# Kernel tuning notes

Measured on AMD Instinct MI355X. Metric: run time of the kernel, lower is better.

Reference implementation:

```python
import jax, jax.numpy as jnp
import numpy as np

H = 16
D = 1024
DK = D // H


def setup_inputs() -> dict:
    key = jax.random.key(0)
    ks = jax.random.split(key, 10)
    B, S = 2, 2048
    scale = 1.0 / np.sqrt(D)
    inp = {
        "query": jax.random.normal(ks[0], (B, S, D), jnp.float32),
        "key_": jax.random.normal(ks[1], (B, S, D), jnp.float32),
        "value": jax.random.normal(ks[2], (B, S, D), jnp.float32),
        "Wq": jax.random.normal(ks[3], (D, D), jnp.float32) * scale,
        "bq": jnp.zeros((D,), jnp.float32),
        "Wk": jax.random.normal(ks[4], (D, D), jnp.float32) * scale,
        "bk": jnp.zeros((D,), jnp.float32),
        "Wv": jax.random.normal(ks[5], (D, D), jnp.float32) * scale,
        "bv": jnp.zeros((D,), jnp.float32),
        "ln_gamma": jnp.ones((D,), jnp.float32),
        "ln_beta": jnp.zeros((D,), jnp.float32),
    }
    return inp


def reference(query, key_, value, Wq, bq, Wk, bk, Wv, bv, ln_gamma, ln_beta):
    B, S, _ = query.shape
    residual = query
    # projections, split into heads: [B, H, S, DK]
    def proj(x, W, b):
        return (x @ W + b).reshape(B, -1, H, DK).transpose(0, 2, 1, 3)
    q = proj(query, Wq, bq)
    k = proj(key_, Wk, bk)
    v = proj(value, Wv, bv)
    # scaled dot-product attention with full score matrix (as in source)
    scores = jnp.einsum("bhqd,bhkd->bhqk", q, k) / jnp.sqrt(jnp.float32(DK))
    p_att = jax.nn.softmax(scores, axis=-1)  # dropout p=0 -> identity
    x = jnp.einsum("bhqk,bhkd->bhqd", p_att, v)
    x = x.transpose(0, 2, 1, 3).reshape(B, S, D)
    # residual + LayerNorm(eps=1e-6)
    y = x + residual
    mu = jnp.mean(y, axis=-1, keepdims=True)
    var = jnp.var(y, axis=-1, keepdims=True)
    y = (y - mu) / jnp.sqrt(var + 1e-6)
    return y * ln_gamma + ln_beta
```

## Files before the change

### kernel.cpp

```cpp
#include <hip/hip_runtime.h>


typedef float f32x4 __attribute__((ext_vector_type(4)));
typedef short short8 __attribute__((ext_vector_type(8)));
typedef unsigned int uint32x2 __attribute__((ext_vector_type(2)));

__device__ __forceinline__ unsigned short f2bf(float f) {
    unsigned u = __builtin_bit_cast(unsigned, f);
    u += 0x7fffu + ((u >> 16) & 1u);
    return (unsigned short)(u >> 16);
}
__device__ __forceinline__ unsigned packbf2(float lo, float hi) {
    return __builtin_amdgcn_perm(__builtin_bit_cast(unsigned, hi),
                                 __builtin_bit_cast(unsigned, lo), 0x07060302u);
}

__device__ __forceinline__ void g2l16(const unsigned short* g, unsigned short* l) {
    __builtin_amdgcn_global_load_lds(
        (const __attribute__((address_space(1))) unsigned int*)g,
        (__attribute__((address_space(3))) unsigned int*)l, 16, 0, 0);
}

__global__ __launch_bounds__(256) void convert_x(
    const float* __restrict__ xq, const float* __restrict__ xk, const float* __restrict__ xv,
    unsigned short* __restrict__ out)
{
    const int z = blockIdx.z;
    const float* src = (z == 0) ? xq : (z == 1) ? xk : xv;
    const size_t idx = ((size_t)blockIdx.x * 256 + threadIdx.x) * 8;
    const float4 a = *(const float4*)(src + idx);
    const float4 b = *(const float4*)(src + idx + 4);
    short8 o;
    o[0] = (short)f2bf(a.x); o[1] = (short)f2bf(a.y);
    o[2] = (short)f2bf(a.z); o[3] = (short)f2bf(a.w);
    o[4] = (short)f2bf(b.x); o[5] = (short)f2bf(b.y);
    o[6] = (short)f2bf(b.z); o[7] = (short)f2bf(b.w);
    *(short8*)(out + (size_t)z * 4194304 + idx) = o;
}

__global__ __launch_bounds__(256) void convert_wt(
    const float* __restrict__ Wq, const float* __restrict__ Wk, const float* __restrict__ Wv,
    unsigned short* __restrict__ out)
{
    const int z = blockIdx.z;
    const float* W = (z == 0) ? Wq : (z == 1) ? Wk : Wv;
    unsigned short* Wt = out + (size_t)z * 1048576;

    __shared__ unsigned short Ts[64 * 65];
    const int tid = threadIdx.x;
    const int kb0 = blockIdx.x * 64, nb0 = blockIdx.y * 64;
    const int a = tid >> 6, b = tid & 63;

#pragma unroll
    for (int i = 0; i < 16; ++i) {
        const int k = i * 4 + a, n = b;
        Ts[n * 65 + k] = f2bf(W[(size_t)(kb0 + k) * 1024 + nb0 + n]);
    }
    __syncthreads();
#pragma unroll
    for (int i = 0; i < 16; ++i) {
        const int n = i * 4 + a, k = b;
        Wt[(size_t)(nb0 + n) * 1024 + kb0 + k] = Ts[n * 65 + k];
    }
}

__global__ __launch_bounds__(256) void qkv_gemm(
    const unsigned short* __restrict__ Xb, const unsigned short* __restrict__ Wtb,
    const float* __restrict__ bq, const float* __restrict__ bk, const float* __restrict__ bv,
    unsigned short* __restrict__ qo, unsigned short* __restrict__ ko, unsigned short* __restrict__ vo)
{
    const int z = blockIdx.z;
    const unsigned short* X  = Xb  + (size_t)z * 4194304;
    const unsigned short* Wt = Wtb + (size_t)z * 1048576;
    const float* bias   = (z == 0) ? bq : (z == 1) ? bk : bv;
    unsigned short* out = (z == 0) ? qo : (z == 1) ? ko : vo;

    __shared__ unsigned short smem[8192];
    unsigned short* As = smem;
    unsigned short* Bs = smem + 4096;

    const int tid  = threadIdx.x;
    const int wave = tid >> 6;
    const int lane = tid & 63;
    const int l15  = lane & 15;
    const int quad = lane >> 4;
    const int mq   = wave & 1, nq = wave >> 1;
    const int mbase = blockIdx.x * 128, nbase = blockIdx.y * 128;

    const int srow = lane >> 2;
    const int schk = (lane & 3) ^ (srow & 3);

    f32x4 acc[4][4];
#pragma unroll
    for (int i = 0; i < 4; ++i)
#pragma unroll
        for (int j = 0; j < 4; ++j) acc[i][j] = (f32x4){0.f, 0.f, 0.f, 0.f};

    for (int k0 = 0; k0 < 1024; k0 += 32) {
        __syncthreads();
#pragma unroll
        for (int t = 0; t < 2; ++t) {
            const int row = wave * 32 + t * 16 + srow;
            g2l16(X  + (size_t)(mbase + row) * 1024 + k0 + schk * 8, &As[(wave * 32 + t * 16) * 32]);
            g2l16(Wt + (size_t)(nbase + row) * 1024 + k0 + schk * 8, &Bs[(wave * 32 + t * 16) * 32]);
        }
        __syncthreads();

        short8 af[4], bf[4];
#pragma unroll
        for (int i = 0; i < 4; ++i) {
            af[i] = *(const short8*)(&As[(mq * 64 + i * 16 + l15) * 32 + ((quad ^ (l15 & 3)) << 3)]);
            bf[i] = *(const short8*)(&Bs[(nq * 64 + i * 16 + l15) * 32 + ((quad ^ (l15 & 3)) << 3)]);
        }
#pragma unroll
        for (int mt = 0; mt < 4; ++mt)
#pragma unroll
            for (int nt = 0; nt < 4; ++nt)
                acc[mt][nt] = __builtin_amdgcn_mfma_f32_16x16x32_bf16(af[mt], bf[nt], acc[mt][nt], 0, 0, 0);
    }

    __syncthreads();

    float bvals[4];
#pragma unroll
    for (int nt = 0; nt < 4; ++nt) bvals[nt] = bias[nbase + nq * 64 + nt * 16 + l15];

    if (z == 2) {
        unsigned short* Epv = smem;
        const int hbase = nbase >> 6;
        const int b     = mbase >> 11;
        const int srow0 = mbase & 2047;
#pragma unroll
        for (int nt = 0; nt < 4; ++nt) {
            __syncthreads();
            short8 w[2];
#pragma unroll
            for (int e = 0; e < 2; ++e)
#pragma unroll
                for (int j = 0; j < 8; ++j) {
                    const int idx = e * 8 + j, mt2 = idx & 3, r = idx >> 2;
                    w[e][j] = (short)f2bf(acc[mt2][nt][r] + bvals[nt]);
                }
            unsigned short* dst = &Epv[(nq * 16 + l15) * 136 + mq * 64 + quad * 16];
            *(short8*)(dst)     = w[0];
            *(short8*)(dst + 8) = w[1];
            __syncthreads();
            const int row = tid >> 3;
            const int d   = nt * 16 + (row & 15);
            const int h   = hbase + (row >> 4);
#pragma unroll
            for (int e = 0; e < 2; ++e) {
                const int colb = e * 64 + (tid & 7) * 8;
                short8 v = *(const short8*)(&Epv[row * 136 + colb]);
                *(short8*)(&out[((size_t)(b * 16 + h) * 64 + d) * 2048 + srow0 + colb]) = v;
            }
        }
    } else {
        unsigned short* Ep = smem + wave * 1152;
        const int hQ = (nbase + nq * 64) >> 6;
        const float scl = (z == 0) ? 0.18033688f : 1.0f;
#pragma unroll
        for (int mt = 0; mt < 4; ++mt) {
#pragma unroll
            for (int nt = 0; nt < 4; ++nt)
#pragma unroll
                for (int r = 0; r < 4; ++r)
                    Ep[(quad * 4 + r) * 72 + nt * 16 + l15] =
                        f2bf((acc[mt][nt][r] + bvals[nt]) * scl);
#pragma unroll
            for (int half = 0; half < 2; ++half) {
                const int m = (lane >> 3) + half * 8;
                const int nblk = lane & 7;
                short8 v = *(const short8*)(&Ep[m * 72 + nblk * 8]);
                const int gm = mbase + mq * 64 + mt * 16 + m;
                const int b2 = gm >> 11, srw = gm & 2047;
                *(short8*)(&out[((size_t)(b2 * 16 + hQ) * 2048 + srw) * 64 + nblk * 8]) = v;
            }
        }
    }
}

__global__ __launch_bounds__(256) void attn(
    const unsigned short* __restrict__ qb, const unsigned short* __restrict__ kb,
    const unsigned short* __restrict__ vtb, float* __restrict__ xw)
{
    const int tid  = threadIdx.x;
    const int wave = tid >> 6;
    const int lane = tid & 63;
    const int l15  = lane & 15;
    const int quad = lane >> 4;

    const int bh    = blockIdx.x;
    const int qbase = blockIdx.y * 128 + wave * 32;

    __shared__ unsigned short Ks[2][64 * 64];
    __shared__ unsigned short Vs[2][64 * 64];
    __shared__ unsigned short Pt[4][2][16][72];

    short8 qf[2][2];
#pragma unroll
    for (int mt = 0; mt < 2; ++mt) {
        const unsigned short* Qp = qb + ((size_t)bh * 2048 + qbase + mt * 16 + l15) * 64 + quad * 8;
        qf[mt][0] = *(const short8*)(Qp);
        qf[mt][1] = *(const short8*)(Qp + 32);
    }

    const unsigned short* Kbh = kb  + (size_t)bh * 2048 * 64;
    const unsigned short* Vbh = vtb + (size_t)bh * 64 * 2048;

    const int r8 = lane >> 3, c8 = lane & 7;
    const unsigned short *srcK[2], *srcV[2];
#pragma unroll
    for (int t = 0; t < 2; ++t) {
        const int row = wave * 16 + t * 8 + r8;
        srcK[t] = Kbh + (size_t)row * 64   + ((c8 ^ r8) << 3);
        srcV[t] = Vbh + (size_t)row * 2048 + ((c8 ^ r8) << 3);
    }

    float l_r[2][4] = {{0.f,0.f,0.f,0.f},{0.f,0.f,0.f,0.f}};
    f32x4 O[2][4];
#pragma unroll
    for (int mt = 0; mt < 2; ++mt)
#pragma unroll
        for (int i = 0; i < 4; ++i) O[mt][i] = (f32x4){0.f, 0.f, 0.f, 0.f};

#pragma unroll
    for (int t = 0; t < 2; ++t) {
        g2l16(srcK[t],      &Ks[0][(wave * 16 + t * 8) * 64]);
        g2l16(srcV[t],      &Vs[0][(wave * 16 + t * 8) * 64]);
    }

    for (int it = 0; it < 32; ++it) {
        const int buf = it & 1;
        __syncthreads();

        if (it + 1 < 32) {
            const size_t kn = (size_t)(it + 1) * 64;
#pragma unroll
            for (int t = 0; t < 2; ++t) {
                g2l16(srcK[t] + kn * 64, &Ks[buf ^ 1][(wave * 16 + t * 8) * 64]);
                g2l16(srcV[t] + kn,      &Vs[buf ^ 1][(wave * 16 + t * 8) * 64]);
            }
        }

        short8 kf[4][2];
#pragma unroll
        for (int ct = 0; ct < 4; ++ct)
#pragma unroll
            for (int kk = 0; kk < 2; ++kk)
                kf[ct][kk] = *(const short8*)(&Ks[buf][(ct * 16 + l15) * 64 +
                                                  ((((kk << 2) + quad) ^ (l15 & 7)) << 3)]);

#pragma unroll
        for (int mt = 0; mt < 2; ++mt) {
            f32x4 sc[4];
#pragma unroll
            for (int ct = 0; ct < 4; ++ct) {
                f32x4 a = {0.f, 0.f, 0.f, 0.f};
                a = __builtin_amdgcn_mfma_f32_16x16x32_bf16(qf[mt][0], kf[ct][0], a, 0, 0, 0);
                a = __builtin_amdgcn_mfma_f32_16x16x32_bf16(qf[mt][1], kf[ct][1], a, 0, 0, 0);
                sc[ct] = a;
            }
#pragma unroll
            for (int r = 0; r < 4; ++r) {
                const float p0 = __builtin_amdgcn_exp2f(sc[0][r]);
                const float p1 = __builtin_amdgcn_exp2f(sc[1][r]);
                const float p2 = __builtin_amdgcn_exp2f(sc[2][r]);
                const float p3 = __builtin_amdgcn_exp2f(sc[3][r]);
                l_r[mt][r] += (p0 + p1) + (p2 + p3);
                uint32x2 pk = {packbf2(p0, p1), packbf2(p2, p3)};
                *(uint32x2*)(&Pt[wave][mt][quad * 4 + r][l15 * 4]) = pk;
            }
        }

#pragma unroll
        for (int c = 0; c < 2; ++c) {
            const short8 pf0 = *(const short8*)(&Pt[wave][0][l15][c * 32 + quad * 8]);
            const short8 pf1 = *(const short8*)(&Pt[wave][1][l15][c * 32 + quad * 8]);
#pragma unroll
            for (int ct4 = 0; ct4 < 4; ++ct4) {
                const short8 vf = *(const short8*)(&Vs[buf][(ct4 * 16 + l15) * 64 +
                                                       ((((c << 2) + quad) ^ (l15 & 7)) << 3)]);
                O[0][ct4] = __builtin_amdgcn_mfma_f32_16x16x32_bf16(pf0, vf, O[0][ct4], 0, 0, 0);
                O[1][ct4] = __builtin_amdgcn_mfma_f32_16x16x32_bf16(pf1, vf, O[1][ct4], 0, 0, 0);
            }
        }
    }

    float inv[2][4];
#pragma unroll
    for (int mt = 0; mt < 2; ++mt)
#pragma unroll
        for (int r = 0; r < 4; ++r) {
            float s = l_r[mt][r];
#pragma unroll
            for (int off = 8; off >= 1; off >>= 1) s += __shfl_xor(s, off);
            inv[mt][r] = 1.0f / s;
        }

    const int b = bh >> 4, h = bh & 15;
#pragma unroll
    for (int mt = 0; mt < 2; ++mt)
#pragma unroll
        for (int ct4 = 0; ct4 < 4; ++ct4)
#pragma unroll
            for (int r = 0; r < 4; ++r) {
                const int s = qbase + mt * 16 + quad * 4 + r;
                xw[((size_t)b * 2048 + s) * 1024 + h * 64 + ct4 * 16 + l15] =
                    O[mt][ct4][r] * inv[mt][r];
            }
}

__global__ __launch_bounds__(256) void ln_kernel(
    const float* __restrict__ xw, const float* __restrict__ res,
    const float* __restrict__ gamma, const float* __restrict__ beta,
    float* __restrict__ out)
{
    const int row = blockIdx.x;
    const int tid = threadIdx.x;
    const size_t base = (size_t)row * 1024 + tid * 4;

    const float4 x  = *(const float4*)(xw + base);
    const float4 rv = *(const float4*)(res + base);
    float4 y;
    y.x = x.x + rv.x; y.y = x.y + rv.y; y.z = x.z + rv.z; y.w = x.w + rv.w;

    float s  = y.x + y.y + y.z + y.w;
    float s2 = y.x * y.x + y.y * y.y + y.z * y.z + y.w * y.w;
#pragma unroll
    for (int off = 32; off >= 1; off >>= 1) {
        s  += __shfl_xor(s, off);
        s2 += __shfl_xor(s2, off);
    }
    __shared__ float red[8];
    const int wave = tid >> 6;
    if ((tid & 63) == 0) { red[wave] = s; red[4 + wave] = s2; }
    __syncthreads();
    s  = red[0] + red[1] + red[2] + red[3];
    s2 = red[4] + red[5] + red[6] + red[7];

    const float mu   = s * (1.0f / 1024.0f);
    const float var  = s2 * (1.0f / 1024.0f) - mu * mu;
    const float rstd = rsqrtf(var + 1e-6f);

    const float4 g  = *(const float4*)(gamma + tid * 4);
    const float4 bt = *(const float4*)(beta + tid * 4);
    float4 o;
    o.x = (y.x - mu) * rstd * g.x + bt.x;
    o.y = (y.y - mu) * rstd * g.y + bt.y;
    o.z = (y.z - mu) * rstd * g.z + bt.z;
    o.w = (y.w - mu) * rstd * g.w + bt.w;
    *(float4*)(out + base) = o;
}

extern "C" void kernel_launch(void* const* d_in, const int* in_sizes, int n_in,
                              void* d_out, int out_size, void* d_ws, size_t ws_size,
                              hipStream_t stream) {
    const float* query = (const float*)d_in[0];
    const float* key_  = (const float*)d_in[1];
    const float* value = (const float*)d_in[2];
    const float* Wq    = (const float*)d_in[3];
    const float* bq    = (const float*)d_in[4];
    const float* Wk    = (const float*)d_in[5];
    const float* bk    = (const float*)d_in[6];
    const float* Wv    = (const float*)d_in[7];
    const float* bv    = (const float*)d_in[8];
    const float* ln_g  = (const float*)d_in[9];
    const float* ln_b  = (const float*)d_in[10];
    float* out = (float*)d_out;

    char* ws = (char*)d_ws;
    unsigned short* Xbuf = (unsigned short*)(ws);
    float*          xwp  = (float*)(ws);
    unsigned short* Wtb  = (unsigned short*)(ws + (size_t)24 * 1024 * 1024);
    unsigned short* qbuf = (unsigned short*)(ws + (size_t)30 * 1024 * 1024);
    unsigned short* kbuf = (unsigned short*)(ws + (size_t)38 * 1024 * 1024);
    unsigned short* vtb  = (unsigned short*)(ws + (size_t)46 * 1024 * 1024);

    convert_x <<<dim3(2048, 1, 3), 256, 0, stream>>>(query, key_, value, Xbuf);
    convert_wt<<<dim3(16, 16, 3),  256, 0, stream>>>(Wq, Wk, Wv, Wtb);
    qkv_gemm  <<<dim3(32, 8, 3),   256, 0, stream>>>(Xbuf, Wtb, bq, bk, bv, qbuf, kbuf, vtb);
    attn      <<<dim3(32, 16),     256, 0, stream>>>(qbuf, kbuf, vtb, xwp);
    ln_kernel <<<4096,             256, 0, stream>>>(xwp, query, ln_g, ln_b, out);
}
```

Before: 220.9 us.

## Double-buffer QKV GEMM LDS tiles and merge conversion kernels into one launch

The QKV projection GEMM now double-buffers its LDS tiles: the next K-slice is prefetched into the alternate buffer right after one barrier per iteration, replacing the two barriers and serialized load/compute of before. The separate input-cast and weight transpose-cast kernels are merged into one launch that dispatches on block index. This targets load latency in the GEMM main loop and one kernel launch gap. It doubles the GEMM's shared memory, which may reduce occupancy.

```diff
diff --git a/kernel.cpp b/kernel.cpp
--- a/kernel.cpp
+++ b/kernel.cpp
@@ -21,46 +21,44 @@
         (__attribute__((address_space(3))) unsigned int*)l, 16, 0, 0);
 }
 
-__global__ __launch_bounds__(256) void convert_x(
+__global__ __launch_bounds__(256) void convert_all(
     const float* __restrict__ xq, const float* __restrict__ xk, const float* __restrict__ xv,
-    unsigned short* __restrict__ out)
+    const float* __restrict__ Wq, const float* __restrict__ Wk, const float* __restrict__ Wv,
+    unsigned short* __restrict__ xout, unsigned short* __restrict__ wout)
 {
-    const int z = blockIdx.z;
-    const float* src = (z == 0) ? xq : (z == 1) ? xk : xv;
-    const size_t idx = ((size_t)blockIdx.x * 256 + threadIdx.x) * 8;
-    const float4 a = *(const float4*)(src + idx);
-    const float4 b = *(const float4*)(src + idx + 4);
-    short8 o;
-    o[0] = (short)f2bf(a.x); o[1] = (short)f2bf(a.y);
-    o[2] = (short)f2bf(a.z); o[3] = (short)f2bf(a.w);
-    o[4] = (short)f2bf(b.x); o[5] = (short)f2bf(b.y);
-    o[6] = (short)f2bf(b.z); o[7] = (short)f2bf(b.w);
-    *(short8*)(out + (size_t)z * 4194304 + idx) = o;
-}
-
-__global__ __launch_bounds__(256) void convert_wt(
-    const float* __restrict__ Wq, const float* __restrict__ Wk, const float* __restrict__ Wv,
-    unsigned short* __restrict__ out)
-{
-    const int z = blockIdx.z;
-    const float* W = (z == 0) ? Wq : (z == 1) ? Wk : Wv;
-    unsigned short* Wt = out + (size_t)z * 1048576;
-
-    __shared__ unsigned short Ts[64 * 65];
+    const int bx  = blockIdx.x;
     const int tid = threadIdx.x;
-    const int kb0 = blockIdx.x * 64, nb0 = blockIdx.y * 64;
-    const int a = tid >> 6, b = tid & 63;
-
-#pragma unroll
-    for (int i = 0; i < 16; ++i) {
-        const int k = i * 4 + a, n = b;
-        Ts[n * 65 + k] = f2bf(W[(size_t)(kb0 + k) * 1024 + nb0 + n]);
-    }
-    __syncthreads();
-#pragma unroll
-    for (int i = 0; i < 16; ++i) {
-        const int n = i * 4 + a, k = b;
-        Wt[(size_t)(nb0 + n) * 1024 + kb0 + k] = Ts[n * 65 + k];
+    if (bx < 6144) {
+        const int z = bx >> 11;
+        const float* src = (z == 0) ? xq : (z == 1) ? xk : xv;
+        const size_t idx = ((size_t)(bx & 2047) * 256 + tid) * 8;
+        const float4 a = *(const float4*)(src + idx);
+        const float4 b = *(const float4*)(src + idx + 4);
+        short8 o;
+        o[0] = (short)f2bf(a.x); o[1] = (short)f2bf(a.y);
+        o[2] = (short)f2bf(a.z); o[3] = (short)f2bf(a.w);
+        o[4] = (short)f2bf(b.x); o[5] = (short)f2bf(b.y);
+        o[6] = (short)f2bf(b.z); o[7] = (short)f2bf(b.w);
+        *(short8*)(xout + (size_t)z * 4194304 + idx) = o;
+    } else {
+        const int i = bx - 6144;
+        const int z = i >> 8, tile = i & 255;
+        const float* W = (z == 0) ? Wq : (z == 1) ? Wk : Wv;
+        unsigned short* Wt = wout + (size_t)z * 1048576;
+        __shared__ unsigned short Ts[64 * 65];
+        const int kb0 = (tile >> 4) * 64, nb0 = (tile & 15) * 64;
+        const int a = tid >> 6, b = tid & 63;
+#pragma unroll
+        for (int j = 0; j < 16; ++j) {
+            const int k = j * 4 + a, n = b;
+            Ts[n * 65 + k] = f2bf(W[(size_t)(kb0 + k) * 1024 + nb0 + n]);
+        }
+        __syncthreads();
+#pragma unroll
+        for (int j = 0; j < 16; ++j) {
+            const int n = j * 4 + a, k = b;
+            Wt[(size_t)(nb0 + n) * 1024 + kb0 + k] = Ts[n * 65 + k];
+        }
     }
 }
 
@@ -75,9 +73,7 @@
     const float* bias   = (z == 0) ? bq : (z == 1) ? bk : bv;
     unsigned short* out = (z == 0) ? qo : (z == 1) ? ko : vo;
 
-    __shared__ unsigned short smem[8192];
-    unsigned short* As = smem;
-    unsigned short* Bs = smem + 4096;
+    __shared__ unsigned short smem[16384];
 
     const int tid  = threadIdx.x;
     const int wave = tid >> 6;
@@ -90,27 +86,40 @@
     const int srow = lane >> 2;
     const int schk = (lane & 3) ^ (srow & 3);
 
+    const unsigned short* srcA = X  + (size_t)(mbase + wave * 32 + srow) * 1024 + schk * 8;
+    const unsigned short* srcB = Wt + (size_t)(nbase + wave * 32 + srow) * 1024 + schk * 8;
+
     f32x4 acc[4][4];
 #pragma unroll
     for (int i = 0; i < 4; ++i)
 #pragma unroll
         for (int j = 0; j < 4; ++j) acc[i][j] = (f32x4){0.f, 0.f, 0.f, 0.f};
 
-    for (int k0 = 0; k0 < 1024; k0 += 32) {
+#pragma unroll
+    for (int t = 0; t < 2; ++t) {
+        g2l16(srcA + (size_t)t * 16 * 1024, &smem[(wave * 32 + t * 16) * 32]);
+        g2l16(srcB + (size_t)t * 16 * 1024, &smem[4096 + (wave * 32 + t * 16) * 32]);
+    }
+
+    for (int it = 0; it < 32; ++it) {
+        const int boff = (it & 1) * 8192;
         __syncthreads();
-#pragma unroll
-        for (int t = 0; t < 2; ++t) {
-            const int row = wave * 32 + t * 16 + srow;
-            g2l16(X  + (size_t)(mbase + row) * 1024 + k0 + schk * 8, &As[(wave * 32 + t * 16) * 32]);
-            g2l16(Wt + (size_t)(nbase + row) * 1024 + k0 + schk * 8, &Bs[(wave * 32 + t * 16) * 32]);
-        }
-        __syncthreads();
+
+        if (it + 1 < 32) {
+            const int poff = boff ^ 8192;
+            const size_t ko2 = (size_t)(it + 1) * 32;
+#pragma unroll
+            for (int t = 0; t < 2; ++t) {
+                g2l16(srcA + (size_t)t * 16 * 1024 + ko2, &smem[poff + (wave * 32 + t * 16) * 32]);
+                g2l16(srcB + (size_t)t * 16 * 1024 + ko2, &smem[poff + 4096 + (wave * 32 + t * 16) * 32]);
+            }
+        }
 
         short8 af[4], bf[4];
 #pragma unroll
         for (int i = 0; i < 4; ++i) {
-            af[i] = *(const short8*)(&As[(mq * 64 + i * 16 + l15) * 32 + ((quad ^ (l15 & 3)) << 3)]);
-            bf[i] = *(const short8*)(&Bs[(nq * 64 + i * 16 + l15) * 32 + ((quad ^ (l15 & 3)) << 3)]);
+            af[i] = *(const short8*)(&smem[boff + (mq * 64 + i * 16 + l15) * 32 + ((quad ^ (l15 & 3)) << 3)]);
+            bf[i] = *(const short8*)(&smem[boff + 4096 + (nq * 64 + i * 16 + l15) * 32 + ((quad ^ (l15 & 3)) << 3)]);
         }
 #pragma unroll
         for (int mt = 0; mt < 4; ++mt)
@@ -226,8 +235,8 @@
 
 #pragma unroll
     for (int t = 0; t < 2; ++t) {
-        g2l16(srcK[t],      &Ks[0][(wave * 16 + t * 8) * 64]);
-        g2l16(srcV[t],      &Vs[0][(wave * 16 + t * 8) * 64]);
+        g2l16(srcK[t], &Ks[0][(wave * 16 + t * 8) * 64]);
+        g2l16(srcV[t], &Vs[0][(wave * 16 + t * 8) * 64]);
     }
 
     for (int it = 0; it < 32; ++it) {
@@ -369,17 +378,17 @@
     const float* ln_b  = (const float*)d_in[10];
     float* out = (float*)d_out;
 
+    const size_t MB = 1024 * 1024;
     char* ws = (char*)d_ws;
     unsigned short* Xbuf = (unsigned short*)(ws);
     float*          xwp  = (float*)(ws);
-    unsigned short* Wtb  = (unsigned short*)(ws + (size_t)24 * 1024 * 1024);
-    unsigned short* qbuf = (unsigned short*)(ws + (size_t)30 * 1024 * 1024);
-    unsigned short* kbuf = (unsigned short*)(ws + (size_t)38 * 1024 * 1024);
-    unsigned short* vtb  = (unsigned short*)(ws + (size_t)46 * 1024 * 1024);
-
-    convert_x <<<dim3(2048, 1, 3), 256, 0, stream>>>(query, key_, value, Xbuf);
-    convert_wt<<<dim3(16, 16, 3),  256, 0, stream>>>(Wq, Wk, Wv, Wtb);
-    qkv_gemm  <<<dim3(32, 8, 3),   256, 0, stream>>>(Xbuf, Wtb, bq, bk, bv, qbuf, kbuf, vtb);
-    attn      <<<dim3(32, 16),     256, 0, stream>>>(qbuf, kbuf, vtb, xwp);
-    ln_kernel <<<4096,             256, 0, stream>>>(xwp, query, ln_g, ln_b, out);
-}
+    unsigned short* Wtb  = (unsigned short*)(ws + 24 * MB);
+    unsigned short* qbuf = (unsigned short*)(ws + 30 * MB);
+    unsigned short* kbuf = (unsigned short*)(ws + 38 * MB);
+    unsigned short* vtb  = (unsigned short*)(ws + 46 * MB);
+
+    convert_all<<<6912,           256, 0, stream>>>(query, key_, value, Wq, Wk, Wv, Xbuf, Wtb);
+    qkv_gemm   <<<dim3(32, 8, 3), 256, 0, stream>>>(Xbuf, Wtb, bq, bk, bv, qbuf, kbuf, vtb);
+    attn       <<<dim3(32, 16),   256, 0, stream>>>(qbuf, kbuf, vtb, xwp);
+    ln_kernel  <<<4096,           256, 0, stream>>>(xwp, query, ln_g, ln_b, out);
+}
```

New measurement: 211.2 us. -4.4%, faster.
